# Optimization experiments

Hardware: AMD Instinct MI355X
Metric: run time of the kernel (lower is better)

Reference implementation:

```python
import jax, jax.numpy as jnp
import numpy as np

MARGIN = 0.1
EPS = 1e-8  # torch CosineSimilarity eps


def setup_inputs() -> dict:
    key = jax.random.key(0)
    k1, k2 = jax.random.split(key)
    embeddings = jax.random.normal(k1, (8192, 128), dtype=jnp.float32)
    labels = jax.random.randint(k2, (8192,), 0, 100, dtype=jnp.int64 if jax.config.jax_enable_x64 else jnp.int32)
    return {"embeddings": embeddings, "labels": labels}


def reference(embeddings, labels):
    n = embeddings.shape[0]
    # Normalize rows (torch: x / max(||x||, eps))
    norm = jnp.linalg.norm(embeddings, axis=1, keepdims=True)
    en = embeddings / jnp.maximum(norm, EPS)
    # Full cosine-similarity matrix via one GEMM: [n, n]
    sim = jnp.einsum('id,jd->ij', en, en)
    same = labels[:, None] == labels[None, :]
    pair_loss = jnp.where(same, jax.nn.relu(1.0 - sim), jax.nn.relu(sim - MARGIN))
    # Sum over i < j (strict upper triangle), matching the double loop
    upper = jnp.triu(jnp.ones((n, n), dtype=pair_loss.dtype), k=1)
    loss = jnp.sum(pair_loss * upper) / (n * (n - 1))
    return loss
```

## Files before the change

kernel.cpp:

```cpp
#include <hip/hip_runtime.h>
#include <hip/hip_bf16.h>


typedef __attribute__((ext_vector_type(8))) short short8;
typedef __attribute__((ext_vector_type(4))) float f32x4;

#define DIM 128
#define MARGIN 0.1f
#define CHUNK 4

typedef const void __attribute__((address_space(1)))* gas_ptr;
typedef void __attribute__((address_space(3)))* las_ptr;

static __device__ __forceinline__ void load16_to_lds(const void* g, void* l) {
    __builtin_amdgcn_global_load_lds((gas_ptr)g, (las_ptr)l, 16, 0, 0);
}

static __device__ __forceinline__ unsigned short f2bf(float f) {
    unsigned int u = __builtin_bit_cast(unsigned int, f);
    u += 0x7FFFu + ((u >> 16) & 1u);
    return (unsigned short)(u >> 16);
}

static __device__ __forceinline__ void stage_tile(const short* __restrict__ en, int row0,
                                                  short* buf, int tid) {
    const char* src = (const char*)(en + (size_t)row0 * DIM);
    char* dst = (char*)buf;
    const int r_lo = tid >> 4;
    const int s    = tid & 15;
    #pragma unroll
    for (int p = 0; p < 8; ++p) {
        const int r  = p * 16 + r_lo;
        const int sc = (s ^ (r & 7)) << 4;
        load16_to_lds(src + (size_t)r * 256 + sc, dst + r * 256 + s * 16);
    }
}

static __device__ __forceinline__ short8 read_frag(const short* buf, int row, int slot) {
    const int ps = slot ^ (row & 7);
    return *(const short8*)(buf + row * DIM + ps * 8);
}

__global__ void __launch_bounds__(256) norm_bf16_kernel(const float* __restrict__ e,
                                                        unsigned int* __restrict__ en_packed) {
    const int row  = blockIdx.x * 4 + (threadIdx.x >> 6);
    const int lane = threadIdx.x & 63;
    const float2 v = *reinterpret_cast<const float2*>(e + row * DIM + lane * 2);
    float s = v.x * v.x + v.y * v.y;
    #pragma unroll
    for (int off = 32; off; off >>= 1) s += __shfl_xor(s, off, 64);
    const float scale = 1.0f / fmaxf(sqrtf(s), 1e-8f);
    const unsigned int lo = f2bf(v.x * scale);
    const unsigned int hi = f2bf(v.y * scale);
    en_packed[row * (DIM / 2) + lane] = (hi << 16) | lo;
}

__global__ void __launch_bounds__(256, 2)
tri_loss_kernel(const short* __restrict__ en, const int* __restrict__ labels,
                float* __restrict__ partials, int nt) {
    __shared__ __align__(16) short buf[2][128 * DIM];
    __shared__ float wsum[4];

    int t  = blockIdx.x;
    int bi = 0, cnt = (nt + CHUNK - 1) / CHUNK;
    #pragma unroll 1
    while (t >= cnt) { t -= cnt; ++bi; cnt = (nt - bi + CHUNK - 1) / CHUNK; }
    const int jbase = bi + t * CHUNK;
    const int ntile = min(CHUNK, nt - jbase);

    const int tid  = threadIdx.x;
    const int lane = tid & 63;
    const int wid  = tid >> 6;
    const int wr   = wid >> 1, wc = wid & 1;
    const int lm   = lane & 15;
    const int hi   = lane >> 4;

    stage_tile(en, bi * 128, &buf[0][0], tid);
    stage_tile(en, jbase * 128, &buf[1][0], tid);

    const int r0 = bi * 128 + wr * 64;
    int4 li[4];
    #pragma unroll
    for (int m = 0; m < 4; ++m) li[m] = *(const int4*)(labels + r0 + m * 16 + hi * 4);

    __syncthreads();

    short8 a[4][4];
    #pragma unroll
    for (int m = 0; m < 4; ++m)
        #pragma unroll
        for (int ks = 0; ks < 4; ++ks)
            a[m][ks] = read_frag(&buf[0][0], wr * 64 + m * 16 + lm, hi + ks * 4);

    __syncthreads();

    float lsum0 = 0.0f, lsum1 = 0.0f;
    const int rb = hi * 4;

    #pragma unroll 1
    for (int tt = 0; tt < ntile; ++tt) {
        const short* cur = &buf[(tt & 1) ^ 1][0];
        if (tt + 1 < ntile)
            stage_tile(en, (jbase + tt + 1) * 128, &buf[tt & 1][0], tid);

        const int bj = jbase + tt;
        const int c0 = bj * 128 + wc * 64;
        int labj[4];
        #pragma unroll
        for (int n = 0; n < 4; ++n) labj[n] = labels[c0 + n * 16 + lm];

        f32x4 acc[4][4] = {};
        #pragma unroll
        for (int ks = 0; ks < 4; ++ks) {
            short8 b[4];
            #pragma unroll
            for (int n = 0; n < 4; ++n)
                b[n] = read_frag(cur, wc * 64 + n * 16 + lm, hi + ks * 4);
            #pragma unroll
            for (int m = 0; m < 4; ++m)
                #pragma unroll
                for (int n = 0; n < 4; ++n)
                    acc[m][n] = __builtin_amdgcn_mfma_f32_16x16x32_bf16(a[m][ks], b[n], acc[m][n], 0, 0, 0);
        }

        const bool diag = (bj == bi);
        #pragma unroll
        for (int m = 0; m < 4; ++m) {
            #pragma unroll
            for (int r = 0; r < 4; ++r) {
                const int i   = r0 + m * 16 + rb + r;
                const int l_i = ((const int*)&li[m])[r];
                #pragma unroll
                for (int n = 0; n < 4; ++n) {
                    const int j  = c0 + n * 16 + lm;
                    const float s  = acc[m][n][r];
                    const float t2 = (l_i == labj[n]) ? (1.0f - s) : (s - MARGIN);
                    const float v  = fmaxf(t2, 0.0f);
                    if (!diag || i < j) { if (n & 1) lsum1 += v; else lsum0 += v; }
                }
            }
        }
        __syncthreads();
    }

    float lsum = lsum0 + lsum1;
    #pragma unroll
    for (int off = 32; off; off >>= 1) lsum += __shfl_down(lsum, off, 64);
    if (lane == 0) wsum[wid] = lsum;
    __syncthreads();
    if (tid == 0) partials[blockIdx.x] = wsum[0] + wsum[1] + wsum[2] + wsum[3];
}

__global__ void __launch_bounds__(256) final_reduce_kernel(const float* __restrict__ partials,
                                                           float* __restrict__ out,
                                                           int n, float inv_denom) {
    float s = 0.0f;
    for (int i = threadIdx.x; i < n; i += 256) s += partials[i];
    #pragma unroll
    for (int off = 32; off; off >>= 1) s += __shfl_xor(s, off, 64);
    __shared__ float wsum[4];
    if ((threadIdx.x & 63) == 0) wsum[threadIdx.x >> 6] = s;
    __syncthreads();
    if (threadIdx.x == 0) out[0] = (wsum[0] + wsum[1] + wsum[2] + wsum[3]) * inv_denom;
}

extern "C" void kernel_launch(void* const* d_in, const int* in_sizes, int n_in,
                              void* d_out, int out_size, void* d_ws, size_t ws_size,
                              hipStream_t stream) {
    const float* emb    = (const float*)d_in[0];
    const int*   labels = (const int*)d_in[1];
    float*       out    = (float*)d_out;

    const int n  = in_sizes[1];
    const int nt = n / 128;

    int Tc = 0;
    for (int i = 0; i < nt; ++i) Tc += (nt - i + CHUNK - 1) / CHUNK;

    unsigned int* en_packed = (unsigned int*)d_ws;
    short*        en        = (short*)d_ws;
    float*        partials  = (float*)((char*)d_ws + (size_t)n * DIM * 2);

    norm_bf16_kernel<<<n / 4, 256, 0, stream>>>(emb, en_packed);

    tri_loss_kernel<<<Tc, 256, 0, stream>>>(en, labels, partials, nt);

    const float inv_denom = (float)(1.0 / ((double)n * (double)(n - 1)));
    final_reduce_kernel<<<1, 256, 0, stream>>>(partials, out, Tc, inv_denom);
}
```

Before: 35.27 us.

## Halve LDS staging tiles to 64 rows and raise occupancy to three blocks

The column-tile pipeline now stages 64-row sub-tiles instead of 128-row tiles, so LDS use drops from 64 KB to 32 KB per block. Each wave computes a 64x32 output patch per step instead of 64x64, halving the accumulator registers, and launch bounds ask for three blocks per SIMD group. The A operand is also staged as two 64-row halves that each wave row-group reads from its own buffer. The trade-off is twice as many loop iterations and barriers, and less MFMA work between each sync.

```diff
diff --git a/kernel.cpp b/kernel.cpp
--- a/kernel.cpp
+++ b/kernel.cpp
@@ -22,14 +22,14 @@
     return (unsigned short)(u >> 16);
 }
 
-static __device__ __forceinline__ void stage_tile(const short* __restrict__ en, int row0,
-                                                  short* buf, int tid) {
+static __device__ __forceinline__ void stage64(const short* __restrict__ en, int row0,
+                                               short* buf, int tid) {
     const char* src = (const char*)(en + (size_t)row0 * DIM);
     char* dst = (char*)buf;
     const int r_lo = tid >> 4;
     const int s    = tid & 15;
     #pragma unroll
-    for (int p = 0; p < 8; ++p) {
+    for (int p = 0; p < 4; ++p) {
         const int r  = p * 16 + r_lo;
         const int sc = (s ^ (r & 7)) << 4;
         load16_to_lds(src + (size_t)r * 256 + sc, dst + r * 256 + s * 16);
@@ -55,10 +55,10 @@
     en_packed[row * (DIM / 2) + lane] = (hi << 16) | lo;
 }
 
-__global__ void __launch_bounds__(256, 2)
+__global__ void __launch_bounds__(256, 3)
 tri_loss_kernel(const short* __restrict__ en, const int* __restrict__ labels,
                 float* __restrict__ partials, int nt) {
-    __shared__ __align__(16) short buf[2][128 * DIM];
+    __shared__ __align__(16) short buf[2][64 * DIM];
     __shared__ float wsum[4];
 
     int t  = blockIdx.x;
@@ -66,7 +66,7 @@
     #pragma unroll 1
     while (t >= cnt) { t -= cnt; ++bi; cnt = (nt - bi + CHUNK - 1) / CHUNK; }
     const int jbase = bi + t * CHUNK;
-    const int ntile = min(CHUNK, nt - jbase);
+    const int nsub  = 2 * min(CHUNK, nt - jbase);
 
     const int tid  = threadIdx.x;
     const int lane = tid & 63;
@@ -75,75 +75,76 @@
     const int lm   = lane & 15;
     const int hi   = lane >> 4;
 
-    stage_tile(en, bi * 128, &buf[0][0], tid);
-    stage_tile(en, jbase * 128, &buf[1][0], tid);
+    stage64(en, bi * 128,      &buf[0][0], tid);
+    stage64(en, bi * 128 + 64, &buf[1][0], tid);
 
-    const int r0 = bi * 128 + wr * 64;
+    const int r0w = bi * 128 + wr * 64;
     int4 li[4];
     #pragma unroll
-    for (int m = 0; m < 4; ++m) li[m] = *(const int4*)(labels + r0 + m * 16 + hi * 4);
+    for (int m = 0; m < 4; ++m) li[m] = *(const int4*)(labels + r0w + m * 16 + hi * 4);
 
     __syncthreads();
 
     short8 a[4][4];
+    const short* Abuf = &buf[wr][0];
     #pragma unroll
     for (int m = 0; m < 4; ++m)
         #pragma unroll
         for (int ks = 0; ks < 4; ++ks)
-            a[m][ks] = read_frag(&buf[0][0], wr * 64 + m * 16 + lm, hi + ks * 4);
+            a[m][ks] = read_frag(Abuf, m * 16 + lm, hi + ks * 4);
 
     __syncthreads();
 
-    float lsum0 = 0.0f, lsum1 = 0.0f;
+    stage64(en, jbase * 128, &buf[0][0], tid);
+    __syncthreads();
+
+    float lsum = 0.0f;
     const int rb = hi * 4;
 
     #pragma unroll 1
-    for (int tt = 0; tt < ntile; ++tt) {
-        const short* cur = &buf[(tt & 1) ^ 1][0];
-        if (tt + 1 < ntile)
-            stage_tile(en, (jbase + tt + 1) * 128, &buf[tt & 1][0], tid);
+    for (int s = 0; s < nsub; ++s) {
+        const short* cur = &buf[s & 1][0];
+        if (s + 1 < nsub)
+            stage64(en, jbase * 128 + (s + 1) * 64, &buf[(s + 1) & 1][0], tid);
 
-        const int bj = jbase + tt;
-        const int c0 = bj * 128 + wc * 64;
-        int labj[4];
-        #pragma unroll
-        for (int n = 0; n < 4; ++n) labj[n] = labels[c0 + n * 16 + lm];
+        const int c0 = jbase * 128 + s * 64 + wc * 32;
+        int labj[2];
+        labj[0] = labels[c0 + lm];
+        labj[1] = labels[c0 + 16 + lm];
 
-        f32x4 acc[4][4] = {};
+        f32x4 acc[4][2] = {};
         #pragma unroll
         for (int ks = 0; ks < 4; ++ks) {
-            short8 b[4];
-            #pragma unroll
-            for (int n = 0; n < 4; ++n)
-                b[n] = read_frag(cur, wc * 64 + n * 16 + lm, hi + ks * 4);
+            short8 b[2];
+            b[0] = read_frag(cur, wc * 32 + lm,      hi + ks * 4);
+            b[1] = read_frag(cur, wc * 32 + 16 + lm, hi + ks * 4);
             #pragma unroll
             for (int m = 0; m < 4; ++m)
                 #pragma unroll
-                for (int n = 0; n < 4; ++n)
+                for (int n = 0; n < 2; ++n)
                     acc[m][n] = __builtin_amdgcn_mfma_f32_16x16x32_bf16(a[m][ks], b[n], acc[m][n], 0, 0, 0);
         }
 
-        const bool diag = (bj == bi);
+        const bool diag = (jbase == bi) && (s < 2);
         #pragma unroll
         for (int m = 0; m < 4; ++m) {
             #pragma unroll
             for (int r = 0; r < 4; ++r) {
-                const int i   = r0 + m * 16 + rb + r;
+                const int i   = r0w + m * 16 + rb + r;
                 const int l_i = ((const int*)&li[m])[r];
                 #pragma unroll
-                for (int n = 0; n < 4; ++n) {
+                for (int n = 0; n < 2; ++n) {
                     const int j  = c0 + n * 16 + lm;
-                    const float s  = acc[m][n][r];
-                    const float t2 = (l_i == labj[n]) ? (1.0f - s) : (s - MARGIN);
+                    const float sv = acc[m][n][r];
+                    const float t2 = (l_i == labj[n]) ? (1.0f - sv) : (sv - MARGIN);
                     const float v  = fmaxf(t2, 0.0f);
-                    if (!diag || i < j) { if (n & 1) lsum1 += v; else lsum0 += v; }
+                    if (!diag || i < j) lsum += v;
                 }
             }
         }
         __syncthreads();
     }
 
-    float lsum = lsum0 + lsum1;
     #pragma unroll
     for (int off = 32; off; off >>= 1) lsum += __shfl_down(lsum, off, 64);
     if (lane == 0) wsum[wid] = lsum;
```

Measured after the change: 31.00 us. -12.1%, faster.
